# Kernel tuning notes

Measured on AMD Instinct MI355X. Metric: run time of the kernel, lower is better.

Reference implementation:

```python
import jax, jax.numpy as jnp
import numpy as np

B, P, L = 8, 196, 80
DIM1, DIM2, ATT = 2048, 300, 1024


def setup_inputs() -> dict:
    key = jax.random.key(0)
    ks = jax.random.split(key, 8)
    s1 = 1.0 / np.sqrt(DIM1)
    s2 = 1.0 / np.sqrt(DIM2)
    sa = 1.0 / np.sqrt(ATT)
    return {
        "x1": jax.random.normal(ks[0], (B, P, DIM1), dtype=jnp.float32),
        "x2": jax.random.normal(ks[1], (B, L, DIM2), dtype=jnp.float32),
        "W1": jax.random.uniform(ks[2], (DIM1, ATT), jnp.float32, -s1, s1),
        "W2": jax.random.uniform(ks[3], (DIM2, ATT), jnp.float32, -s2, s2),
        "Wh": jax.random.uniform(ks[4], (ATT, ATT), jnp.float32, -sa, sa),
        "bh": jax.random.uniform(ks[5], (ATT,), jnp.float32, -sa, sa),
        "Wt": jax.random.uniform(ks[6], (ATT,), jnp.float32, -sa, sa),
        "bt": jax.random.uniform(ks[7], (), jnp.float32, -sa, sa),
    }


def reference(x1, x2, W1, W2, Wh, bh, Wt, bt):
    # linear1 / linear2 (no bias)
    a1 = jnp.einsum('bpd,da->bpa', x1, W1)            # (B, P, ATT)
    a2 = jnp.einsum('bld,da->bla', x2, W2)            # (B, L, ATT)
    u = jnp.tanh(a1[:, None, :, :] * a2[:, :, None, :])  # (B, L, P, ATT)
    # target_linear(hidden_linear(u)) folded: u @ (Wh @ Wt) + (bh @ Wt + bt)
    w = Wh @ Wt                                        # (ATT,)
    score = jnp.einsum('blpa,a->blp', u, w) + (bh @ Wt + bt)  # (B, L, P)
    alpha = jax.nn.softmax(score, axis=-1)             # (B, L, P)
    label_repr = jnp.einsum('blp,bpd->bld', alpha, x1)  # (B, L, DIM1)
    return (label_repr, alpha)
```

## Files before the change

### kernel.cpp

```cpp
#include <hip/hip_runtime.h>
#include <math.h>

#define B_   8
#define P_   196
#define L_   80
#define DIM1 2048
#define DIM2 300
#define ATT  1024

typedef __attribute__((ext_vector_type(8))) short short8_t;
typedef __attribute__((ext_vector_type(4))) float f32x4_t;

__device__ inline unsigned short f2bf(float f) {
    unsigned int u = __float_as_uint(f);
    u += 0x7fff + ((u >> 16) & 1);
    return (unsigned short)(u >> 16);
}
__device__ inline float bf2f(unsigned short h) {
    return __uint_as_float(((unsigned int)h) << 16);
}

__global__ __launch_bounds__(256) void prep_w(const float* __restrict__ Wh,
                                              const float* __restrict__ bh,
                                              const float* __restrict__ Wt,
                                              const float* __restrict__ btp,
                                              float* __restrict__ w,
                                              float* __restrict__ biasp) {
    const int tid  = threadIdx.x;
    const int lane = tid & 63;
    const int row  = blockIdx.x * 4 + (tid >> 6);
    const float* src = (row < ATT) ? (Wh + (size_t)row * ATT) : bh;
    if (row <= ATT) {
        float acc = 0.0f;
#pragma unroll
        for (int it = 0; it < ATT / 256; ++it) {
            const int i = it * 256 + lane * 4;
            const float4 a = *reinterpret_cast<const float4*>(src + i);
            const float4 b = *reinterpret_cast<const float4*>(Wt + i);
            acc = fmaf(a.x, b.x, acc);
            acc = fmaf(a.y, b.y, acc);
            acc = fmaf(a.z, b.z, acc);
            acc = fmaf(a.w, b.w, acc);
        }
#pragma unroll
        for (int o = 32; o >= 1; o >>= 1) acc += __shfl_xor(acc, o);
        if (lane == 0) {
            if (row < ATT) w[row] = acc;
            else           biasp[0] = acc + btp[0];
        }
    }
}

__global__ __launch_bounds__(256) void prep_sum(const float* __restrict__ w,
                                                float* __restrict__ biasp) {
    __shared__ float red[4];
    const int tid = threadIdx.x;
    float s = 0.f;
    for (int i = tid; i < ATT; i += 256) s += w[i];
#pragma unroll
    for (int o = 32; o >= 1; o >>= 1) s += __shfl_xor(s, o);
    if ((tid & 63) == 0) red[tid >> 6] = s;
    __syncthreads();
    if (tid == 0) biasp[1] = biasp[0] + red[0] + red[1] + red[2] + red[3];
}

__global__ __launch_bounds__(256) void tcast(const float* __restrict__ in,
                                             unsigned short* __restrict__ out,
                                             int Ksrc, int Kpad) {
    __shared__ unsigned short tile[32][34];
    const int tx = threadIdx.x & 31, ty = threadIdx.x >> 5;
    const int k0 = blockIdx.x * 32, n0 = blockIdx.y * 32;
#pragma unroll
    for (int i = 0; i < 4; ++i) {
        const int r = k0 + ty + i * 8;
        const float v = (r < Ksrc) ? in[(size_t)r * 1024 + n0 + tx] : 0.f;
        tile[ty + i * 8][tx] = f2bf(v);
    }
    __syncthreads();
#pragma unroll
    for (int i = 0; i < 4; ++i) {
        const int n = ty + i * 8;
        out[(size_t)(n0 + n) * Kpad + k0 + tx] = tile[tx][n];
    }
}

template<int KSRC, int KPAD>
__global__ __launch_bounds__(256) void gemm_bf16(const float* __restrict__ Af,
                                                 const unsigned short* __restrict__ Bt,
                                                 unsigned short* __restrict__ C,
                                                 int M) {
    constexpr int NT = KPAD / 64;
    __shared__ __align__(16) char smem[32768];
    const int tid  = threadIdx.x;
    const int lane = tid & 63;
    const int wave = tid >> 6;
    const int wm = (wave >> 1) * 32;
    const int wn = (wave & 1) * 32;
    const int m0 = blockIdx.y * 64;
    const int n0 = blockIdx.x * 64;

    const int row = tid >> 2;
    const int kc  = (tid & 3) * 16;
    const int swz = (row & 7) << 4;
    const int sb  = row * 128 + kc * 2;
    const int gm  = m0 + row;

    float4   ra[4];
    short8_t rb[2];

    auto LOAD = [&](int t) {
        const int k0 = t * 64;
        if (gm < M && k0 + 64 <= KSRC) {
            const float* ap = Af + (size_t)gm * KSRC + k0 + kc;
            ra[0] = *reinterpret_cast<const float4*>(ap);
            ra[1] = *reinterpret_cast<const float4*>(ap + 4);
            ra[2] = *reinterpret_cast<const float4*>(ap + 8);
            ra[3] = *reinterpret_cast<const float4*>(ap + 12);
        } else {
            float* rf = reinterpret_cast<float*>(ra);
#pragma unroll
            for (int j = 0; j < 16; ++j) {
                const int k = k0 + kc + j;
                rf[j] = (gm < M && k < KSRC) ? Af[(size_t)gm * KSRC + k] : 0.f;
            }
        }
        const unsigned short* bp = Bt + (size_t)(n0 + row) * KPAD + k0 + kc;
        rb[0] = *reinterpret_cast<const short8_t*>(bp);
        rb[1] = *reinterpret_cast<const short8_t*>(bp + 8);
    };

    auto WRITE = [&](int buf) {
        char* smA = smem + buf * 16384;
        char* smB = smA + 8192;
        const float* rf = reinterpret_cast<const float*>(ra);
        short8_t h0, h1;
#pragma unroll
        for (int j = 0; j < 8; ++j) h0[j] = (short)f2bf(rf[j]);
#pragma unroll
        for (int j = 0; j < 8; ++j) h1[j] = (short)f2bf(rf[8 + j]);
        *reinterpret_cast<short8_t*>(smA + ((sb)      ^ swz)) = h0;
        *reinterpret_cast<short8_t*>(smA + ((sb + 16) ^ swz)) = h1;
        *reinterpret_cast<short8_t*>(smB + ((sb)      ^ swz)) = rb[0];
        *reinterpret_cast<short8_t*>(smB + ((sb + 16) ^ swz)) = rb[1];
    };

    f32x4_t acc[2][2] = {};
    const int fr_col = (lane >> 4) << 4;
    const int fl     = lane & 15;

    LOAD(0);
#pragma unroll 2
    for (int t = 0; t < NT; ++t) {
        const int buf = t & 1;
        WRITE(buf);
        __syncthreads();
        if (t + 1 < NT) LOAD(t + 1);
        const char* smA = smem + buf * 16384;
        const char* smB = smA + 8192;
#pragma unroll
        for (int kk = 0; kk < 2; ++kk) {
            short8_t af[2], bf[2];
#pragma unroll
            for (int i = 0; i < 2; ++i) {
                const int r = wm + i * 16 + fl;
                af[i] = *reinterpret_cast<const short8_t*>(
                    smA + ((r * 128 + kk * 64 + fr_col) ^ ((r & 7) << 4)));
            }
#pragma unroll
            for (int j = 0; j < 2; ++j) {
                const int r = wn + j * 16 + fl;
                bf[j] = *reinterpret_cast<const short8_t*>(
                    smB + ((r * 128 + kk * 64 + fr_col) ^ ((r & 7) << 4)));
            }
#pragma unroll
            for (int i = 0; i < 2; ++i)
#pragma unroll
                for (int j = 0; j < 2; ++j)
                    acc[i][j] = __builtin_amdgcn_mfma_f32_16x16x32_bf16(af[i], bf[j], acc[i][j], 0, 0, 0);
        }
        __syncthreads();
    }

#pragma unroll
    for (int i = 0; i < 2; ++i) {
        const int gmb = m0 + wm + i * 16 + ((lane >> 4) << 2);
#pragma unroll
        for (int j = 0; j < 2; ++j) {
            const int gn = n0 + wn + j * 16 + fl;
#pragma unroll
            for (int q = 0; q < 4; ++q) {
                const int gmq = gmb + q;
                if (gmq < M) C[(size_t)gmq * 1024 + gn] = f2bf(acc[i][j][q]);
            }
        }
    }
}

__global__ __launch_bounds__(256) void score_softmax(const unsigned short* __restrict__ a1b,
                                                     const unsigned short* __restrict__ a2b,
                                                     const float* __restrict__ w,
                                                     const float* __restrict__ biasp,
                                                     float* __restrict__ alpha) {
    __shared__ float2 aw[ATT];
    __shared__ float sc[P_];
    __shared__ float red[4];
    const int tid  = threadIdx.x;
    const int lane = tid & 63;
    const int wave = tid >> 6;
    const int b = blockIdx.x & 7;
    const int l = blockIdx.x >> 3;
    const float bias2 = biasp[1];

    const unsigned short* a2p = a2b + (size_t)(b * L_ + l) * ATT;
    for (int i = tid; i < ATT; i += 256) {
        const float a2v = bf2f(a2p[i]);
        const int li = i & 511;
        const int phi = (i & ~511) | (((li & 7) << 6) + (li >> 3));
        aw[phi] = make_float2(a2v * 2.885390082f, w[i]);
    }
    __syncthreads();

    for (int p0 = wave * 4; p0 < P_; p0 += 16) {
        const unsigned short* a1p = a1b + (size_t)(b * P_ + p0) * ATT;
        float acc[4] = {0.f, 0.f, 0.f, 0.f};
#pragma unroll
        for (int it = 0; it < 2; ++it) {
            short8_t v[4];
#pragma unroll
            for (int q = 0; q < 4; ++q)
                v[q] = *reinterpret_cast<const short8_t*>(a1p + q * ATT + it * 512 + lane * 8);
#pragma unroll
            for (int j = 0; j < 8; ++j) {
                const float2 c = aw[it * 512 + j * 64 + lane];
#pragma unroll
                for (int q = 0; q < 4; ++q) {
                    const float f = bf2f((unsigned short)v[q][j]);
                    const float e = __builtin_amdgcn_exp2f(f * c.x);
                    const float r = __builtin_amdgcn_rcpf(e + 1.0f);
                    acc[q] = fmaf(c.y, r, acc[q]);
                }
            }
        }
#pragma unroll
        for (int o = 32; o >= 1; o >>= 1) {
#pragma unroll
            for (int q = 0; q < 4; ++q) acc[q] += __shfl_xor(acc[q], o);
        }
        if (lane < 4) sc[p0 + lane] = bias2 - 2.0f * acc[lane];
    }
    __syncthreads();

    const float v = (tid < P_) ? sc[tid] : -INFINITY;
    float m = v;
#pragma unroll
    for (int o = 32; o >= 1; o >>= 1) m = fmaxf(m, __shfl_xor(m, o));
    if (lane == 0) red[wave] = m;
    __syncthreads();
    m = fmaxf(fmaxf(red[0], red[1]), fmaxf(red[2], red[3]));

    const float e = (tid < P_) ? __expf(v - m) : 0.0f;
    float s = e;
#pragma unroll
    for (int o = 32; o >= 1; o >>= 1) s += __shfl_xor(s, o);
    __syncthreads();
    if (lane == 0) red[wave] = s;
    __syncthreads();
    s = red[0] + red[1] + red[2] + red[3];

    if (tid < P_) alpha[(size_t)(b * L_ + l) * P_ + tid] = e / s;
}

#define LT 4
#define DT 512
__global__ __launch_bounds__(256) void label_kernel(const float* __restrict__ alpha,
                                                    const float* __restrict__ x1,
                                                    float* __restrict__ out) {
    __shared__ float al[P_][LT];
    const int tid = threadIdx.x;
    const int b  = blockIdx.z;
    const int l0 = blockIdx.y * LT;
    const int d0 = blockIdx.x * DT;

    for (int idx = tid; idx < P_ * LT; idx += 256) {
        const int p = idx >> 2;
        const int l = idx & 3;
        al[p][l] = alpha[((size_t)(b * L_ + l0 + l)) * P_ + p];
    }
    __syncthreads();

    const int d = d0 + tid * 2;
    float acc[LT][2] = {};
    for (int p = 0; p < P_; ++p) {
        const float2 x = *reinterpret_cast<const float2*>(x1 + ((size_t)(b * P_ + p)) * DIM1 + d);
        const float4 a4 = *reinterpret_cast<const float4*>(&al[p][0]);
        acc[0][0] = fmaf(a4.x, x.x, acc[0][0]);
        acc[0][1] = fmaf(a4.x, x.y, acc[0][1]);
        acc[1][0] = fmaf(a4.y, x.x, acc[1][0]);
        acc[1][1] = fmaf(a4.y, x.y, acc[1][1]);
        acc[2][0] = fmaf(a4.z, x.x, acc[2][0]);
        acc[2][1] = fmaf(a4.z, x.y, acc[2][1]);
        acc[3][0] = fmaf(a4.w, x.x, acc[3][0]);
        acc[3][1] = fmaf(a4.w, x.y, acc[3][1]);
    }
#pragma unroll
    for (int l = 0; l < LT; ++l) {
        float* op = out + ((size_t)(b * L_ + l0 + l)) * DIM1 + d;
        op[0] = acc[l][0];
        op[1] = acc[l][1];
    }
}

extern "C" void kernel_launch(void* const* d_in, const int* in_sizes, int n_in,
                              void* d_out, int out_size, void* d_ws, size_t ws_size,
                              hipStream_t stream) {
    const float* x1 = (const float*)d_in[0];
    const float* x2 = (const float*)d_in[1];
    const float* W1 = (const float*)d_in[2];
    const float* W2 = (const float*)d_in[3];
    const float* Wh = (const float*)d_in[4];
    const float* bh = (const float*)d_in[5];
    const float* Wt = (const float*)d_in[6];
    const float* bt = (const float*)d_in[7];

    float* out       = (float*)d_out;
    float* label_out = out;
    float* alpha_out = out + (size_t)B_ * L_ * DIM1;

    unsigned short* usw = (unsigned short*)d_ws;
    unsigned short* W1T = usw;
    unsigned short* a2b = usw;
    unsigned short* W2T = usw + 2097152;
    unsigned short* a1b = usw + 2424832;
    float* wv    = (float*)(usw + 4030464);
    float* biasv = wv + ATT;

    prep_w<<<ATT / 4 + 1, 256, 0, stream>>>(Wh, bh, Wt, bt, wv, biasv);
    prep_sum<<<1, 256, 0, stream>>>(wv, biasv);

    tcast<<<dim3(DIM1 / 32, 32), 256, 0, stream>>>(W1, W1T, DIM1, DIM1);
    tcast<<<dim3(320 / 32, 32), 256, 0, stream>>>(W2, W2T, DIM2, 320);

    gemm_bf16<DIM1, DIM1><<<dim3(16, 25), 256, 0, stream>>>(x1, W1T, a1b, B_ * P_);
    gemm_bf16<DIM2, 320><<<dim3(16, 10), 256, 0, stream>>>(x2, W2T, a2b, B_ * L_);

    score_softmax<<<B_ * L_, 256, 0, stream>>>(a1b, a2b, wv, biasv, alpha_out);

    label_kernel<<<dim3(DIM1 / DT, L_ / LT, B_), 256, 0, stream>>>(
        alpha_out, x1, label_out);
}
```

Baseline: 193.4 us.

## Split score computation across four blocks per row and add separate softmax kernel

The fused score+softmax kernel, which used one block per (b,l) row, is split into a score kernel that uses four blocks per row, each covering 49 of the P positions, followed by a separate softmax kernel with one wave per row. The goal is to raise the grid from 640 to 2560 blocks so the tanh-heavy score phase fills the GPU's compute units better. In exchange it adds an extra launch and a global round trip for scores, and each block repeats the aw staging in shared memory. The last group in each quarter computes clamped padding rows, which is wasted work.

```diff
diff --git a/kernel.cpp b/kernel.cpp
--- a/kernel.cpp
+++ b/kernel.cpp
@@ -196,19 +196,19 @@
     }
 }
 
-__global__ __launch_bounds__(256) void score_softmax(const unsigned short* __restrict__ a1b,
-                                                     const unsigned short* __restrict__ a2b,
-                                                     const float* __restrict__ w,
-                                                     const float* __restrict__ biasp,
-                                                     float* __restrict__ alpha) {
+__global__ __launch_bounds__(256) void score_part(const unsigned short* __restrict__ a1b,
+                                                  const unsigned short* __restrict__ a2b,
+                                                  const float* __restrict__ w,
+                                                  const float* __restrict__ biasp,
+                                                  float* __restrict__ scb) {
     __shared__ float2 aw[ATT];
-    __shared__ float sc[P_];
-    __shared__ float red[4];
     const int tid  = threadIdx.x;
     const int lane = tid & 63;
     const int wave = tid >> 6;
-    const int b = blockIdx.x & 7;
-    const int l = blockIdx.x >> 3;
+    const int b    = blockIdx.x & 7;
+    const int rest = blockIdx.x >> 3;
+    const int l    = rest >> 2;
+    const int qtr  = rest & 3;
     const float bias2 = biasp[1];
 
     const unsigned short* a2p = a2b + (size_t)(b * L_ + l) * ATT;
@@ -220,15 +220,22 @@
     }
     __syncthreads();
 
-    for (int p0 = wave * 4; p0 < P_; p0 += 16) {
-        const unsigned short* a1p = a1b + (size_t)(b * P_ + p0) * ATT;
+    const int base = qtr * 49;
+    float* scp = scb + (size_t)(b * L_ + l) * P_;
+
+    for (int g = wave; g < 13; g += 4) {
+        const int p0 = base + g * 4;
+        int r[4];
+#pragma unroll
+        for (int q = 0; q < 4; ++q) r[q] = min(p0 + q, P_ - 1);
         float acc[4] = {0.f, 0.f, 0.f, 0.f};
 #pragma unroll
         for (int it = 0; it < 2; ++it) {
             short8_t v[4];
 #pragma unroll
             for (int q = 0; q < 4; ++q)
-                v[q] = *reinterpret_cast<const short8_t*>(a1p + q * ATT + it * 512 + lane * 8);
+                v[q] = *reinterpret_cast<const short8_t*>(
+                    a1b + (size_t)(b * P_ + r[q]) * ATT + it * 512 + lane * 8);
 #pragma unroll
             for (int j = 0; j < 8; ++j) {
                 const float2 c = aw[it * 512 + j * 64 + lane];
@@ -236,8 +243,8 @@
                 for (int q = 0; q < 4; ++q) {
                     const float f = bf2f((unsigned short)v[q][j]);
                     const float e = __builtin_amdgcn_exp2f(f * c.x);
-                    const float r = __builtin_amdgcn_rcpf(e + 1.0f);
-                    acc[q] = fmaf(c.y, r, acc[q]);
+                    const float rr = __builtin_amdgcn_rcpf(e + 1.0f);
+                    acc[q] = fmaf(c.y, rr, acc[q]);
                 }
             }
         }
@@ -246,28 +253,49 @@
 #pragma unroll
             for (int q = 0; q < 4; ++q) acc[q] += __shfl_xor(acc[q], o);
         }
-        if (lane < 4) sc[p0 + lane] = bias2 - 2.0f * acc[lane];
-    }
-    __syncthreads();
-
-    const float v = (tid < P_) ? sc[tid] : -INFINITY;
-    float m = v;
+        if (lane < 4) {
+            const int p = p0 + lane;
+            if (p < base + 49) scp[p] = bias2 - 2.0f * acc[lane];
+        }
+    }
+}
+
+__global__ __launch_bounds__(256) void softmax_k(const float* __restrict__ scb,
+                                                 float* __restrict__ alpha) {
+    const int tid  = threadIdx.x;
+    const int lane = tid & 63;
+    const int wave = tid >> 6;
+    const int row  = blockIdx.x * 4 + wave;
+    const float* sp = scb + (size_t)row * P_;
+
+    float v[4];
+#pragma unroll
+    for (int k = 0; k < 4; ++k) {
+        const int p = lane + k * 64;
+        v[k] = (p < P_) ? sp[p] : -INFINITY;
+    }
+    float m = fmaxf(fmaxf(v[0], v[1]), fmaxf(v[2], v[3]));
 #pragma unroll
     for (int o = 32; o >= 1; o >>= 1) m = fmaxf(m, __shfl_xor(m, o));
-    if (lane == 0) red[wave] = m;
-    __syncthreads();
-    m = fmaxf(fmaxf(red[0], red[1]), fmaxf(red[2], red[3]));
-
-    const float e = (tid < P_) ? __expf(v - m) : 0.0f;
-    float s = e;
+
+    float e[4];
+    float s = 0.f;
+#pragma unroll
+    for (int k = 0; k < 4; ++k) {
+        const int p = lane + k * 64;
+        e[k] = (p < P_) ? __expf(v[k] - m) : 0.f;
+        s += e[k];
+    }
 #pragma unroll
     for (int o = 32; o >= 1; o >>= 1) s += __shfl_xor(s, o);
-    __syncthreads();
-    if (lane == 0) red[wave] = s;
-    __syncthreads();
-    s = red[0] + red[1] + red[2] + red[3];
-
-    if (tid < P_) alpha[(size_t)(b * L_ + l) * P_ + tid] = e / s;
+    const float inv = 1.0f / s;
+
+    float* ap = alpha + (size_t)row * P_;
+#pragma unroll
+    for (int k = 0; k < 4; ++k) {
+        const int p = lane + k * 64;
+        if (p < P_) ap[p] = e[k] * inv;
+    }
 }
 
 #define LT 4
@@ -333,6 +361,7 @@
     unsigned short* a1b = usw + 2424832;
     float* wv    = (float*)(usw + 4030464);
     float* biasv = wv + ATT;
+    float* scb   = wv + 1028;
 
     prep_w<<<ATT / 4 + 1, 256, 0, stream>>>(Wh, bh, Wt, bt, wv, biasv);
     prep_sum<<<1, 256, 0, stream>>>(wv, biasv);
@@ -343,7 +372,8 @@
     gemm_bf16<DIM1, DIM1><<<dim3(16, 25), 256, 0, stream>>>(x1, W1T, a1b, B_ * P_);
     gemm_bf16<DIM2, 320><<<dim3(16, 10), 256, 0, stream>>>(x2, W2T, a2b, B_ * L_);
 
-    score_softmax<<<B_ * L_, 256, 0, stream>>>(a1b, a2b, wv, biasv, alpha_out);
+    score_part<<<B_ * L_ * 4, 256, 0, stream>>>(a1b, a2b, wv, biasv, scb);
+    softmax_k<<<B_ * L_ / 4, 256, 0, stream>>>(scb, alpha_out);
 
     label_kernel<<<dim3(DIM1 / DT, L_ / LT, B_), 256, 0, stream>>>(
         alpha_out, x1, label_out);
```

Result: no change. 192.2 us (-0.7%).
